# Performance work log

Measured on AMD Instinct MI355X. Metric: run time of the kernel, lower is better.

The kernel has to match this reference:

```python
import jax, jax.numpy as jnp
import numpy as np

B, C, H, W = 4, 256, 128, 256
CQK = C // 4   # 64
COUT = 256


def setup_inputs() -> dict:
    key = jax.random.key(0)
    ks = jax.random.split(key, 8)
    s = 0.05
    return {
        "flow": jax.random.normal(ks[0], (B, C, H, W), jnp.float32),
        "de_out": jax.random.normal(ks[1], (B, C, H, W), jnp.float32),
        "Wq": jax.random.normal(ks[2], (CQK, C), jnp.float32) * s,
        "bq": jax.random.normal(ks[3], (CQK,), jnp.float32) * s,
        "Wk": jax.random.normal(ks[4], (CQK, C), jnp.float32) * s,
        "bk": jax.random.normal(ks[5], (CQK,), jnp.float32) * s,
        "Wv": jax.random.normal(ks[6], (COUT, C), jnp.float32) * s,
        "bv": jax.random.normal(ks[7], (COUT,), jnp.float32) * s,
    }


def reference(flow, de_out, Wq, bq, Wk, bk, Wv, bv):
    # 1x1 convs == channel-mixing einsums
    q = jnp.einsum('bchw,dc->bdhw', de_out, Wq) + bq[None, :, None, None]  # [B,CQK,H,W]
    k = jnp.einsum('bchw,dc->bdhw', flow, Wk) + bk[None, :, None, None]   # [B,CQK,H,W]
    v = jnp.einsum('bchw,oc->bohw', flow, Wv) + bv[None, :, None, None]   # [B,COUT,H,W]
    # width-axial attention: energy[b,h,w,w'] = sum_d q[b,d,h,w]*k[b,d,h,w']
    energy = jnp.einsum('bdhw,bdhv->bhwv', q, k)          # [B,H,W,W]
    att = jax.nn.softmax(energy, axis=-1)                 # softmax over key width w'
    # out[b,o,h,w] = sum_{w'} v[b,o,h,w'] * att[b,h,w,w']
    out = jnp.einsum('bohv,bhwv->bohw', v, att)           # [B,COUT,H,W]
    return out
```

## Files before the change

kernel.cpp:

```cpp
#include <hip/hip_runtime.h>

#define Bn   4
#define Cc   256
#define Hh   128
#define Ww   256
#define HWp  32768
#define CQK  64
#define COUT 256

typedef _Float16 half8 __attribute__((ext_vector_type(8)));
typedef _Float16 half4 __attribute__((ext_vector_type(4)));
typedef float   floatx4 __attribute__((ext_vector_type(4)));

#define MFMA16(a, b, c) __builtin_amdgcn_mfma_f32_16x16x32_f16((a), (b), (c), 0, 0, 0)

__global__ __launch_bounds__(256) void k_qkv(
    const float* __restrict__ flow, const float* __restrict__ de_out,
    const float* __restrict__ Wq, const float* __restrict__ bq,
    const float* __restrict__ Wk, const float* __restrict__ bk,
    const float* __restrict__ Wv, const float* __restrict__ bv,
    _Float16* __restrict__ Qws, _Float16* __restrict__ Kws,
    _Float16* __restrict__ Vws)
{
    __shared__ __align__(16) _Float16 x_lds[64 * 264];
    __shared__ __align__(16) _Float16 w_lds[32 * 264];

    const int t   = threadIdx.x;
    const int b   = blockIdx.y;
    const int job = blockIdx.z;
    const int pb  = blockIdx.x * 64;

    const float* X = (job == 0 ? de_out : flow) + (size_t)b * Cc * HWp;

    {
        const int px4 = t & 15;
        const int cg  = t >> 4;
        for (int rep = 0; rep < 4; ++rep) {
            const int c0 = 4 * cg + 64 * rep;
            float4 r0 = *(const float4*)&X[(size_t)(c0 + 0) * HWp + pb + 4 * px4];
            float4 r1 = *(const float4*)&X[(size_t)(c0 + 1) * HWp + pb + 4 * px4];
            float4 r2 = *(const float4*)&X[(size_t)(c0 + 2) * HWp + pb + 4 * px4];
            float4 r3 = *(const float4*)&X[(size_t)(c0 + 3) * HWp + pb + 4 * px4];
            half4 h;
            h = (half4){(_Float16)r0.x, (_Float16)r1.x, (_Float16)r2.x, (_Float16)r3.x};
            *(half4*)&x_lds[(4 * px4 + 0) * 264 + c0] = h;
            h = (half4){(_Float16)r0.y, (_Float16)r1.y, (_Float16)r2.y, (_Float16)r3.y};
            *(half4*)&x_lds[(4 * px4 + 1) * 264 + c0] = h;
            h = (half4){(_Float16)r0.z, (_Float16)r1.z, (_Float16)r2.z, (_Float16)r3.z};
            *(half4*)&x_lds[(4 * px4 + 2) * 264 + c0] = h;
            h = (half4){(_Float16)r0.w, (_Float16)r1.w, (_Float16)r2.w, (_Float16)r3.w};
            *(half4*)&x_lds[(4 * px4 + 3) * 264 + c0] = h;
        }
    }

    const int nmt  = (job == 0) ? 2 : 10;
    const int wv   = t >> 6;
    const int lane = t & 63;
    const int quad = lane >> 4;
    const int l16  = lane & 15;

    for (int mt = 0; mt < nmt; ++mt) {
        const float* Wsel;
        const float* bsel;
        int mbase, dstmode;
        _Float16* dst;
        if (job == 0)      { Wsel = Wq; bsel = bq; mbase = mt * 32;        dst = Qws; dstmode = 0; }
        else if (mt < 2)   { Wsel = Wk; bsel = bk; mbase = mt * 32;        dst = Kws; dstmode = 0; }
        else               { Wsel = Wv; bsel = bv; mbase = (mt - 2) * 32;  dst = Vws; dstmode = 1; }

        __syncthreads();
        for (int i = 0; i < 8; ++i) {
            const int f4  = t + 256 * i;
            const int row = f4 >> 6;
            const int off = (f4 & 63) * 4;
            float4 w4 = *(const float4*)&Wsel[(size_t)(mbase + row) * 256 + off];
            half4 h = (half4){(_Float16)w4.x, (_Float16)w4.y, (_Float16)w4.z, (_Float16)w4.w};
            *(half4*)&w_lds[row * 264 + off] = h;
        }
        __syncthreads();

        const int mrow = 16 * (wv & 1) + l16;
        half8 a[8];
        for (int ks = 0; ks < 8; ++ks)
            a[ks] = *(const half8*)&w_lds[mrow * 264 + ks * 32 + quad * 8];

        const int n0 = (wv >> 1) * 32;
        floatx4 acc0 = {0.f, 0.f, 0.f, 0.f};
        floatx4 acc1 = {0.f, 0.f, 0.f, 0.f};
        for (int ks = 0; ks < 8; ++ks) {
            half8 b0 = *(const half8*)&x_lds[(n0 + l16) * 264 + ks * 32 + quad * 8];
            half8 b1 = *(const half8*)&x_lds[(n0 + 16 + l16) * 264 + ks * 32 + quad * 8];
            acc0 = MFMA16(a[ks], b0, acc0);
            acc1 = MFMA16(a[ks], b1, acc1);
        }

        const int mloc = 16 * (wv & 1) + quad * 4;
        float4 bi = *(const float4*)&bsel[mbase + mloc];
        const float bia[4] = {bi.x, bi.y, bi.z, bi.w};
        if (dstmode == 0) {
            for (int nt = 0; nt < 2; ++nt) {
                floatx4 acc = nt ? acc1 : acc0;
                const int pix = pb + n0 + nt * 16 + l16;
                half4 h = (half4){(_Float16)(acc[0] + bia[0]), (_Float16)(acc[1] + bia[1]),
                                  (_Float16)(acc[2] + bia[2]), (_Float16)(acc[3] + bia[3])};
                *(half4*)&dst[((size_t)b * HWp + pix) * 64 + mt * 32 + mloc] = h;
            }
        } else {
            for (int nt = 0; nt < 2; ++nt) {
                floatx4 acc = nt ? acc1 : acc0;
                const int pix = pb + n0 + nt * 16 + l16;
                for (int r = 0; r < 4; ++r) {
                    const int o = mbase + mloc + r;
                    dst[((size_t)b * 256 + o) * HWp + pix] = (_Float16)(acc[r] + bia[r]);
                }
            }
        }
    }
}

__global__ __launch_bounds__(256) void k_attn(
    const _Float16* __restrict__ Qws, const _Float16* __restrict__ Kws,
    const _Float16* __restrict__ Vws, float* __restrict__ out)
{
    __shared__ __align__(16) _Float16 q_lds[32 * 72];
    __shared__ __align__(16) _Float16 k_lds[256 * 72];
    __shared__ __align__(16) _Float16 att_lds[32 * 264];
    __shared__ float inv_l[32];

    const int t    = threadIdx.x;
    const int h    = blockIdx.x;
    const int b    = blockIdx.y;
    const int wv   = t >> 6;
    const int lane = t & 63;
    const int quad = lane >> 4;
    const int l16  = lane & 15;
    const size_t pixbase = (size_t)b * HWp + h * 256;

    for (int chunk = 0; chunk < 8; ++chunk) {
        __syncthreads();
        {
            const int row = t >> 3, off = (t & 7) * 8;
            *(half8*)&q_lds[row * 72 + off] =
                *(const half8*)&Qws[(pixbase + chunk * 32 + row) * 64 + off];
        }
        for (int i = 0; i < 8; ++i) {
            const int g = t + 256 * i;
            const int row = g >> 3, off = (g & 7) * 8;
            *(half8*)&k_lds[row * 72 + off] =
                *(const half8*)&Kws[(pixbase + row) * 64 + off];
        }
        __syncthreads();

        {
            const int mrow = 16 * (wv & 1) + l16;
            half8 a0 = *(const half8*)&q_lds[mrow * 72 + quad * 8];
            half8 a1 = *(const half8*)&q_lds[mrow * 72 + 32 + quad * 8];
            const int mb2 = 16 * (wv & 1) + quad * 4;
            for (int j = 0; j < 8; ++j) {
                const int nt = (wv >> 1) * 8 + j;
                half8 b0 = *(const half8*)&k_lds[(nt * 16 + l16) * 72 + quad * 8];
                half8 b1 = *(const half8*)&k_lds[(nt * 16 + l16) * 72 + 32 + quad * 8];
                floatx4 acc = {0.f, 0.f, 0.f, 0.f};
                acc = MFMA16(a0, b0, acc);
                acc = MFMA16(a1, b1, acc);
                for (int r = 0; r < 4; ++r)
                    att_lds[(mb2 + r) * 264 + nt * 16 + l16] = (_Float16)acc[r];
            }
        }
        __syncthreads();

        {
            const int r = t >> 3, seg = t & 7;
            _Float16* rowp = &att_lds[r * 264 + seg * 32];
            float vals[32];
            float mx = -1e30f;
            for (int i = 0; i < 32; ++i) { vals[i] = (float)rowp[i]; mx = fmaxf(mx, vals[i]); }
            mx = fmaxf(mx, __shfl_xor(mx, 1));
            mx = fmaxf(mx, __shfl_xor(mx, 2));
            mx = fmaxf(mx, __shfl_xor(mx, 4));
            float s = 0.f;
            for (int i = 0; i < 32; ++i) { vals[i] = __expf(vals[i] - mx); s += vals[i]; }
            s += __shfl_xor(s, 1);
            s += __shfl_xor(s, 2);
            s += __shfl_xor(s, 4);
            for (int i = 0; i < 32; ++i) rowp[i] = (_Float16)vals[i];
            if (seg == 0) inv_l[r] = 1.f / s;
        }
        __syncthreads();

        _Float16* v_lds = k_lds;
        for (int os = 0; os < 4; ++os) {
            if (os) __syncthreads();
            for (int i = 0; i < 8; ++i) {
                const int g = t + 256 * i;
                const int row = g >> 5, off = (g & 31) * 8;
                *(half8*)&v_lds[row * 264 + off] =
                    *(const half8*)&Vws[((size_t)b * 256 + os * 64 + row) * HWp + h * 256 + off];
            }
            __syncthreads();

            floatx4 acc0 = {0.f, 0.f, 0.f, 0.f};
            floatx4 acc1 = {0.f, 0.f, 0.f, 0.f};
            for (int ks = 0; ks < 8; ++ks) {
                half8 a  = *(const half8*)&v_lds[(16 * wv + l16) * 264 + ks * 32 + quad * 8];
                half8 b0 = *(const half8*)&att_lds[l16 * 264 + ks * 32 + quad * 8];
                half8 b1 = *(const half8*)&att_lds[(16 + l16) * 264 + ks * 32 + quad * 8];
                acc0 = MFMA16(a, b0, acc0);
                acc1 = MFMA16(a, b1, acc1);
            }
            const float il0 = inv_l[l16];
            const float il1 = inv_l[16 + l16];
            const int og = os * 64 + 16 * wv + quad * 4;
            const int wg = chunk * 32 + l16;
            for (int r = 0; r < 4; ++r) {
                out[(((size_t)b * 256 + og + r) * Hh + h) * Ww + wg]      = acc0[r] * il0;
                out[(((size_t)b * 256 + og + r) * Hh + h) * Ww + 16 + wg] = acc1[r] * il1;
            }
        }
    }
}

extern "C" void kernel_launch(void* const* d_in, const int* in_sizes, int n_in,
                              void* d_out, int out_size, void* d_ws, size_t ws_size,
                              hipStream_t stream)
{
    const float* flow   = (const float*)d_in[0];
    const float* de_out = (const float*)d_in[1];
    const float* Wq = (const float*)d_in[2];
    const float* bq = (const float*)d_in[3];
    const float* Wk = (const float*)d_in[4];
    const float* bk = (const float*)d_in[5];
    const float* Wv = (const float*)d_in[6];
    const float* bv = (const float*)d_in[7];

    _Float16* Qws = (_Float16*)d_ws;
    _Float16* Kws = Qws + (size_t)Bn * HWp * 64;
    _Float16* Vws = Kws + (size_t)Bn * HWp * 64;
    float* out = (float*)d_out;

    dim3 g1(HWp / 64, Bn, 2);
    k_qkv<<<g1, 256, 0, stream>>>(flow, de_out, Wq, bq, Wk, bk, Wv, bv, Qws, Kws, Vws);

    dim3 g2(Hh, Bn);
    k_attn<<<g2, 256, 0, stream>>>(Qws, Kws, Vws, out);
}
```

Baseline: 451.9 us.

## Keep K in LDS and V in registers across chunks; pre-convert weights to fp16

In the attention kernel, K is now staged into LDS once per row and each wave's V fragments are held in registers for all chunks. Previously both were reloaded from global memory on every one of the 8 query chunks. Q fragments are read straight from global memory, and the LDS tiles use XOR swizzling instead of padding. The weights are converted to fp16 once by a small extra kernel into scratch space at the end of the output buffer, so the QKV kernel reads fp16 weights directly with no per-tile LDS staging or barriers. The cost is much higher register pressure in the attention kernel (128 VGPRs for V alone), which may lower occupancy, plus reliance on out_size being in bytes for the scratch placement.

```diff
diff --git a/kernel.cpp b/kernel.cpp
--- a/kernel.cpp
+++ b/kernel.cpp
@@ -14,16 +14,33 @@
 
 #define MFMA16(a, b, c) __builtin_amdgcn_mfma_f32_16x16x32_f16((a), (b), (c), 0, 0, 0)
 
-__global__ __launch_bounds__(256) void k_qkv(
+__global__ __launch_bounds__(256) void k_wcvt(
+    const float* __restrict__ Wq, const float* __restrict__ Wk,
+    const float* __restrict__ Wv, _Float16* __restrict__ W16)
+{
+    const int e = (blockIdx.x * 256 + threadIdx.x) * 8;
+    const float* src;
+    if (e < 16384)      src = Wq + e;
+    else if (e < 32768) src = Wk + (e - 16384);
+    else                src = Wv + (e - 32768);
+    float4 f0 = *(const float4*)src;
+    float4 f1 = *(const float4*)(src + 4);
+    half8 h = {(_Float16)f0.x, (_Float16)f0.y, (_Float16)f0.z, (_Float16)f0.w,
+               (_Float16)f1.x, (_Float16)f1.y, (_Float16)f1.z, (_Float16)f1.w};
+    *(half8*)&W16[e] = h;
+}
+
+__device__ __forceinline__ int xswz(int row) { return ((row ^ (row >> 2)) & 7) << 3; }
+
+__global__ __launch_bounds__(256, 4) void k_qkv(
     const float* __restrict__ flow, const float* __restrict__ de_out,
-    const float* __restrict__ Wq, const float* __restrict__ bq,
-    const float* __restrict__ Wk, const float* __restrict__ bk,
-    const float* __restrict__ Wv, const float* __restrict__ bv,
+    const _Float16* __restrict__ W16,
+    const float* __restrict__ bq, const float* __restrict__ bk,
+    const float* __restrict__ bv,
     _Float16* __restrict__ Qws, _Float16* __restrict__ Kws,
     _Float16* __restrict__ Vws)
 {
-    __shared__ __align__(16) _Float16 x_lds[64 * 264];
-    __shared__ __align__(16) _Float16 w_lds[32 * 264];
+    __shared__ __align__(16) _Float16 x_lds[64 * 256];
 
     const int t   = threadIdx.x;
     const int b   = blockIdx.y;
@@ -35,61 +52,59 @@
     {
         const int px4 = t & 15;
         const int cg  = t >> 4;
+        #pragma unroll
         for (int rep = 0; rep < 4; ++rep) {
             const int c0 = 4 * cg + 64 * rep;
             float4 r0 = *(const float4*)&X[(size_t)(c0 + 0) * HWp + pb + 4 * px4];
             float4 r1 = *(const float4*)&X[(size_t)(c0 + 1) * HWp + pb + 4 * px4];
             float4 r2 = *(const float4*)&X[(size_t)(c0 + 2) * HWp + pb + 4 * px4];
             float4 r3 = *(const float4*)&X[(size_t)(c0 + 3) * HWp + pb + 4 * px4];
+            const int r = 4 * px4;
             half4 h;
             h = (half4){(_Float16)r0.x, (_Float16)r1.x, (_Float16)r2.x, (_Float16)r3.x};
-            *(half4*)&x_lds[(4 * px4 + 0) * 264 + c0] = h;
+            *(half4*)&x_lds[(r + 0) * 256 + (c0 ^ xswz(r + 0))] = h;
             h = (half4){(_Float16)r0.y, (_Float16)r1.y, (_Float16)r2.y, (_Float16)r3.y};
-            *(half4*)&x_lds[(4 * px4 + 1) * 264 + c0] = h;
+            *(half4*)&x_lds[(r + 1) * 256 + (c0 ^ xswz(r + 1))] = h;
             h = (half4){(_Float16)r0.z, (_Float16)r1.z, (_Float16)r2.z, (_Float16)r3.z};
-            *(half4*)&x_lds[(4 * px4 + 2) * 264 + c0] = h;
+            *(half4*)&x_lds[(r + 2) * 256 + (c0 ^ xswz(r + 2))] = h;
             h = (half4){(_Float16)r0.w, (_Float16)r1.w, (_Float16)r2.w, (_Float16)r3.w};
-            *(half4*)&x_lds[(4 * px4 + 3) * 264 + c0] = h;
-        }
-    }
-
-    const int nmt  = (job == 0) ? 2 : 10;
+            *(half4*)&x_lds[(r + 3) * 256 + (c0 ^ xswz(r + 3))] = h;
+        }
+    }
+    __syncthreads();
+
     const int wv   = t >> 6;
     const int lane = t & 63;
     const int quad = lane >> 4;
     const int l16  = lane & 15;
+    const int mrow = 16 * (wv & 1) + l16;
+    const int n0   = (wv >> 1) * 32;
+    const int nmt  = (job == 0) ? 2 : 10;
+
+    const int rowb0 = n0 + l16;
+    const int rowb1 = n0 + 16 + l16;
+    const int sw0 = xswz(rowb0);
+    const int sw1 = xswz(rowb1);
 
     for (int mt = 0; mt < nmt; ++mt) {
-        const float* Wsel;
+        int wbase, mbase, dstmode;
         const float* bsel;
-        int mbase, dstmode;
         _Float16* dst;
-        if (job == 0)      { Wsel = Wq; bsel = bq; mbase = mt * 32;        dst = Qws; dstmode = 0; }
-        else if (mt < 2)   { Wsel = Wk; bsel = bk; mbase = mt * 32;        dst = Kws; dstmode = 0; }
-        else               { Wsel = Wv; bsel = bv; mbase = (mt - 2) * 32;  dst = Vws; dstmode = 1; }
-
-        __syncthreads();
-        for (int i = 0; i < 8; ++i) {
-            const int f4  = t + 256 * i;
-            const int row = f4 >> 6;
-            const int off = (f4 & 63) * 4;
-            float4 w4 = *(const float4*)&Wsel[(size_t)(mbase + row) * 256 + off];
-            half4 h = (half4){(_Float16)w4.x, (_Float16)w4.y, (_Float16)w4.z, (_Float16)w4.w};
-            *(half4*)&w_lds[row * 264 + off] = h;
-        }
-        __syncthreads();
-
-        const int mrow = 16 * (wv & 1) + l16;
+        if (job == 0)     { wbase = 0;         mbase = mt * 32;       bsel = bq; dst = Qws; dstmode = 0; }
+        else if (mt < 2)  { wbase = 64 * 256;  mbase = mt * 32;       bsel = bk; dst = Kws; dstmode = 0; }
+        else              { wbase = 128 * 256; mbase = (mt - 2) * 32; bsel = bv; dst = Vws; dstmode = 1; }
+
         half8 a[8];
+        #pragma unroll
         for (int ks = 0; ks < 8; ++ks)
-            a[ks] = *(const half8*)&w_lds[mrow * 264 + ks * 32 + quad * 8];
-
-        const int n0 = (wv >> 1) * 32;
+            a[ks] = *(const half8*)&W16[wbase + (mbase + mrow) * 256 + ks * 32 + quad * 8];
+
         floatx4 acc0 = {0.f, 0.f, 0.f, 0.f};
         floatx4 acc1 = {0.f, 0.f, 0.f, 0.f};
+        #pragma unroll
         for (int ks = 0; ks < 8; ++ks) {
-            half8 b0 = *(const half8*)&x_lds[(n0 + l16) * 264 + ks * 32 + quad * 8];
-            half8 b1 = *(const half8*)&x_lds[(n0 + 16 + l16) * 264 + ks * 32 + quad * 8];
+            half8 b0 = *(const half8*)&x_lds[rowb0 * 256 + ((ks * 32 + quad * 8) ^ sw0)];
+            half8 b1 = *(const half8*)&x_lds[rowb1 * 256 + ((ks * 32 + quad * 8) ^ sw1)];
             acc0 = MFMA16(a[ks], b0, acc0);
             acc1 = MFMA16(a[ks], b1, acc1);
         }
@@ -98,17 +113,20 @@
         float4 bi = *(const float4*)&bsel[mbase + mloc];
         const float bia[4] = {bi.x, bi.y, bi.z, bi.w};
         if (dstmode == 0) {
+            #pragma unroll
             for (int nt = 0; nt < 2; ++nt) {
                 floatx4 acc = nt ? acc1 : acc0;
                 const int pix = pb + n0 + nt * 16 + l16;
                 half4 h = (half4){(_Float16)(acc[0] + bia[0]), (_Float16)(acc[1] + bia[1]),
                                   (_Float16)(acc[2] + bia[2]), (_Float16)(acc[3] + bia[3])};
-                *(half4*)&dst[((size_t)b * HWp + pix) * 64 + mt * 32 + mloc] = h;
+                *(half4*)&dst[((size_t)b * HWp + pix) * 64 + mbase + mloc] = h;
             }
         } else {
+            #pragma unroll
             for (int nt = 0; nt < 2; ++nt) {
                 floatx4 acc = nt ? acc1 : acc0;
                 const int pix = pb + n0 + nt * 16 + l16;
+                #pragma unroll
                 for (int r = 0; r < 4; ++r) {
                     const int o = mbase + mloc + r;
                     dst[((size_t)b * 256 + o) * HWp + pix] = (_Float16)(acc[r] + bia[r]);
@@ -118,13 +136,12 @@
     }
 }
 
-__global__ __launch_bounds__(256) void k_attn(
+__global__ __launch_bounds__(256, 2) void k_attn(
     const _Float16* __restrict__ Qws, const _Float16* __restrict__ Kws,
     const _Float16* __restrict__ Vws, float* __restrict__ out)
 {
-    __shared__ __align__(16) _Float16 q_lds[32 * 72];
-    __shared__ __align__(16) _Float16 k_lds[256 * 72];
-    __shared__ __align__(16) _Float16 att_lds[32 * 264];
+    __shared__ __align__(16) _Float16 k_lds[256 * 64];
+    __shared__ __align__(16) _Float16 att_lds[32 * 256];
     __shared__ float inv_l[32];
 
     const int t    = threadIdx.x;
@@ -136,85 +153,111 @@
     const int l16  = lane & 15;
     const size_t pixbase = (size_t)b * HWp + h * 256;
 
+    half8 vf[4][8];
+    #pragma unroll
+    for (int os = 0; os < 4; ++os)
+        #pragma unroll
+        for (int ks = 0; ks < 8; ++ks)
+            vf[os][ks] = *(const half8*)&Vws[((size_t)b * 256 + os * 64 + 16 * wv + l16) * HWp
+                                             + h * 256 + ks * 32 + quad * 8];
+
+    #pragma unroll
+    for (int i = 0; i < 8; ++i) {
+        const int g = t + 256 * i;
+        const int row = g >> 3, off = (g & 7) * 8;
+        *(half8*)&k_lds[row * 64 + (off ^ ((row & 7) << 3))] =
+            *(const half8*)&Kws[(pixbase + row) * 64 + off];
+    }
+    __syncthreads();
+
+    const int wt  = wv & 1;
+    const int swq = (l16 & 7) << 3;
+
     for (int chunk = 0; chunk < 8; ++chunk) {
-        __syncthreads();
+        if (chunk) __syncthreads();
+
         {
-            const int row = t >> 3, off = (t & 7) * 8;
-            *(half8*)&q_lds[row * 72 + off] =
-                *(const half8*)&Qws[(pixbase + chunk * 32 + row) * 64 + off];
-        }
-        for (int i = 0; i < 8; ++i) {
-            const int g = t + 256 * i;
-            const int row = g >> 3, off = (g & 7) * 8;
-            *(half8*)&k_lds[row * 72 + off] =
-                *(const half8*)&Kws[(pixbase + row) * 64 + off];
-        }
-        __syncthreads();
-
-        {
-            const int mrow = 16 * (wv & 1) + l16;
-            half8 a0 = *(const half8*)&q_lds[mrow * 72 + quad * 8];
-            half8 a1 = *(const half8*)&q_lds[mrow * 72 + 32 + quad * 8];
-            const int mb2 = 16 * (wv & 1) + quad * 4;
+            const size_t qrow = pixbase + chunk * 32 + wt * 16 + l16;
+            half8 bq0 = *(const half8*)&Qws[qrow * 64 + quad * 8];
+            half8 bq1 = *(const half8*)&Qws[qrow * 64 + 32 + quad * 8];
+            #pragma unroll
             for (int j = 0; j < 8; ++j) {
                 const int nt = (wv >> 1) * 8 + j;
-                half8 b0 = *(const half8*)&k_lds[(nt * 16 + l16) * 72 + quad * 8];
-                half8 b1 = *(const half8*)&k_lds[(nt * 16 + l16) * 72 + 32 + quad * 8];
+                const int krow = nt * 16 + l16;
+                half8 a0 = *(const half8*)&k_lds[krow * 64 + ((quad * 8) ^ swq)];
+                half8 a1 = *(const half8*)&k_lds[krow * 64 + ((32 + quad * 8) ^ swq)];
                 floatx4 acc = {0.f, 0.f, 0.f, 0.f};
-                acc = MFMA16(a0, b0, acc);
-                acc = MFMA16(a1, b1, acc);
-                for (int r = 0; r < 4; ++r)
-                    att_lds[(mb2 + r) * 264 + nt * 16 + l16] = (_Float16)acc[r];
+                acc = MFMA16(a0, bq0, acc);
+                acc = MFMA16(a1, bq1, acc);
+                half4 hv = (half4){(_Float16)acc[0], (_Float16)acc[1],
+                                   (_Float16)acc[2], (_Float16)acc[3]};
+                *(half4*)&att_lds[(wt * 16 + l16) * 256 + ((nt * 16 + quad * 4) ^ swq)] = hv;
             }
         }
         __syncthreads();
 
         {
             const int r = t >> 3, seg = t & 7;
-            _Float16* rowp = &att_lds[r * 264 + seg * 32];
-            float vals[32];
+            const int sw = (r & 7) << 3;
+            _Float16* base = &att_lds[r * 256];
+            half8 v[4];
             float mx = -1e30f;
-            for (int i = 0; i < 32; ++i) { vals[i] = (float)rowp[i]; mx = fmaxf(mx, vals[i]); }
+            #pragma unroll
+            for (int u = 0; u < 4; ++u) {
+                v[u] = *(const half8*)&base[(seg * 32 + u * 8) ^ sw];
+                #pragma unroll
+                for (int e = 0; e < 8; ++e) mx = fmaxf(mx, (float)v[u][e]);
+            }
             mx = fmaxf(mx, __shfl_xor(mx, 1));
             mx = fmaxf(mx, __shfl_xor(mx, 2));
             mx = fmaxf(mx, __shfl_xor(mx, 4));
             float s = 0.f;
-            for (int i = 0; i < 32; ++i) { vals[i] = __expf(vals[i] - mx); s += vals[i]; }
+            #pragma unroll
+            for (int u = 0; u < 4; ++u) {
+                half8 ex;
+                #pragma unroll
+                for (int e = 0; e < 8; ++e) {
+                    const float p = __expf((float)v[u][e] - mx);
+                    s += p;
+                    ex[e] = (_Float16)p;
+                }
+                *(half8*)&base[(seg * 32 + u * 8) ^ sw] = ex;
+            }
             s += __shfl_xor(s, 1);
             s += __shfl_xor(s, 2);
             s += __shfl_xor(s, 4);
-            for (int i = 0; i < 32; ++i) rowp[i] = (_Float16)vals[i];
             if (seg == 0) inv_l[r] = 1.f / s;
         }
         __syncthreads();
 
-        _Float16* v_lds = k_lds;
-        for (int os = 0; os < 4; ++os) {
-            if (os) __syncthreads();
-            for (int i = 0; i < 8; ++i) {
-                const int g = t + 256 * i;
-                const int row = g >> 5, off = (g & 31) * 8;
-                *(half8*)&v_lds[row * 264 + off] =
-                    *(const half8*)&Vws[((size_t)b * 256 + os * 64 + row) * HWp + h * 256 + off];
-            }
-            __syncthreads();
-
-            floatx4 acc0 = {0.f, 0.f, 0.f, 0.f};
-            floatx4 acc1 = {0.f, 0.f, 0.f, 0.f};
+        {
+            floatx4 acc[4][2];
+            #pragma unroll
+            for (int os = 0; os < 4; ++os) {
+                acc[os][0] = (floatx4){0.f, 0.f, 0.f, 0.f};
+                acc[os][1] = (floatx4){0.f, 0.f, 0.f, 0.f};
+            }
+            #pragma unroll
             for (int ks = 0; ks < 8; ++ks) {
-                half8 a  = *(const half8*)&v_lds[(16 * wv + l16) * 264 + ks * 32 + quad * 8];
-                half8 b0 = *(const half8*)&att_lds[l16 * 264 + ks * 32 + quad * 8];
-                half8 b1 = *(const half8*)&att_lds[(16 + l16) * 264 + ks * 32 + quad * 8];
-                acc0 = MFMA16(a, b0, acc0);
-                acc1 = MFMA16(a, b1, acc1);
+                half8 p0 = *(const half8*)&att_lds[l16 * 256 + ((ks * 32 + quad * 8) ^ swq)];
+                half8 p1 = *(const half8*)&att_lds[(16 + l16) * 256 + ((ks * 32 + quad * 8) ^ swq)];
+                #pragma unroll
+                for (int os = 0; os < 4; ++os) {
+                    acc[os][0] = MFMA16(vf[os][ks], p0, acc[os][0]);
+                    acc[os][1] = MFMA16(vf[os][ks], p1, acc[os][1]);
+                }
             }
             const float il0 = inv_l[l16];
             const float il1 = inv_l[16 + l16];
-            const int og = os * 64 + 16 * wv + quad * 4;
             const int wg = chunk * 32 + l16;
-            for (int r = 0; r < 4; ++r) {
-                out[(((size_t)b * 256 + og + r) * Hh + h) * Ww + wg]      = acc0[r] * il0;
-                out[(((size_t)b * 256 + og + r) * Hh + h) * Ww + 16 + wg] = acc1[r] * il1;
+            #pragma unroll
+            for (int os = 0; os < 4; ++os) {
+                const int og = os * 64 + 16 * wv + quad * 4;
+                #pragma unroll
+                for (int r = 0; r < 4; ++r) {
+                    out[(((size_t)b * 256 + og + r) * Hh + h) * Ww + wg]      = acc[os][0][r] * il0;
+                    out[(((size_t)b * 256 + og + r) * Hh + h) * Ww + 16 + wg] = acc[os][1][r] * il1;
+                }
             }
         }
     }
@@ -238,8 +281,12 @@
     _Float16* Vws = Kws + (size_t)Bn * HWp * 64;
     float* out = (float*)d_out;
 
+    _Float16* W16 = (_Float16*)((char*)d_out + (size_t)out_size - 98304 * sizeof(_Float16));
+
+    k_wcvt<<<dim3(48), 256, 0, stream>>>(Wq, Wk, Wv, W16);
+
     dim3 g1(HWp / 64, Bn, 2);
-    k_qkv<<<g1, 256, 0, stream>>>(flow, de_out, Wq, bq, Wk, bk, Wv, bv, Qws, Kws, Vws);
+    k_qkv<<<g1, 256, 0, stream>>>(flow, de_out, W16, bq, bk, bv, Qws, Kws, Vws);
 
     dim3 g2(Hh, Bn);
     k_attn<<<g2, 256, 0, stream>>>(Qws, Kws, Vws, out);
```

Result: faster. 430.2 us (-4.8%).
